# Optimization experiments

Measured on AMD Instinct MI355X. Metric: run time of the kernel, lower is better.

## Reference

```python
import jax, jax.numpy as jnp
import numpy as np

DZ, DA, K, T, BS, H = 32, 16, 3, 128, 512, 128


def setup_inputs() -> dict:
    key = jax.random.key(0)
    ks = jax.random.split(key, 8)
    s = 0.02
    # A/C: identity-like init (as in the torch module) plus small noise, per mixture k and timestep t
    A = jnp.eye(DZ, dtype=jnp.float32) + s * jax.random.normal(ks[0], (K, T, DZ, DZ), jnp.float32)
    C = jnp.eye(DA, DZ, dtype=jnp.float32) + s * jax.random.normal(ks[1], (K, T, DA, DZ), jnp.float32)
    a0 = jnp.zeros((DA,), jnp.float32)
    a = jax.random.normal(ks[2], (BS, T, DA), jnp.float32)

    def lw(k, shape):
        return 0.05 * jax.random.normal(k, shape, jnp.float32)

    Wih0 = lw(ks[3], (4 * H, DA)); Whh0 = lw(ks[4], (4 * H, H))
    bih0 = jnp.zeros((4 * H,), jnp.float32); bhh0 = jnp.zeros((4 * H,), jnp.float32)
    Wih1 = lw(ks[5], (4 * H, H)); Whh1 = lw(ks[6], (4 * H, H))
    bih1 = jnp.zeros((4 * H,), jnp.float32); bhh1 = jnp.zeros((4 * H,), jnp.float32)
    Wlin = lw(ks[7], (K, H)); blin = jnp.zeros((K,), jnp.float32)
    return dict(a=a, A=A, C=C, a0=a0, Wih0=Wih0, Whh0=Whh0, bih0=bih0, bhh0=bhh0,
                Wih1=Wih1, Whh1=Whh1, bih1=bih1, bhh1=bhh1, Wlin=Wlin, blin=blin)


def _lstm_layer(x, Wih, Whh, bih, bhh):
    # x: (bs, L, din) -> (bs, L, H); PyTorch gate order i, f, g, o; zero initial state
    Hd = Whh.shape[1]
    b = bih + bhh

    def step(carry, xt):
        h, c = carry
        g = xt @ Wih.T + h @ Whh.T + b
        i, f, gg, o = jnp.split(g, 4, axis=-1)
        c = jax.nn.sigmoid(f) * c + jax.nn.sigmoid(i) * jnp.tanh(gg)
        h = jax.nn.sigmoid(o) * jnp.tanh(c)
        return (h, c), h

    h0 = jnp.zeros((x.shape[0], Hd), x.dtype)
    _, hs = jax.lax.scan(step, (h0, h0), jnp.swapaxes(x, 0, 1))
    return jnp.swapaxes(hs, 0, 1)


def _filter(a, A, C, a0, Wih0, Whh0, bih0, bhh0, Wih1, Whh1, bih1, bhh1, Wlin, blin):
    bs, L, da = a.shape
    dz = A.shape[-1]
    R = 0.01 * jnp.eye(da, dtype=a.dtype)
    Q = 0.01 * jnp.eye(dz, dtype=a.dtype)

    # dynamics network: alpha_t from [a_0, a_0..a_{L-2}]
    code = jnp.concatenate([jnp.broadcast_to(a0, (bs, 1, da)), a[:, :-1]], axis=1)
    h = _lstm_layer(code, Wih0, Whh0, bih0, bhh0)
    h = _lstm_layer(h, Wih1, Whh1, bih1, bhh1)
    alpha = jax.nn.softmax(h @ Wlin.T + blin, axis=-1)  # (bs, L, K)

    A_mix = jnp.einsum('blk,klij->blij', alpha, A)  # (bs, L, dz, dz)
    C_mix = jnp.einsum('blk,klij->blij', alpha, C)  # (bs, L, da, dz)
    # A is applied at index t+1 for the prediction step; last slot is a dummy (its output is unused)
    A_next = jnp.concatenate([A_mix[:, 1:], A_mix[:, -1:]], axis=1)

    mu0 = jnp.zeros((bs, dz), a.dtype)
    sig0 = jnp.broadcast_to(jnp.eye(dz, dtype=a.dtype), (bs, dz, dz))
    I = jnp.eye(dz, dtype=a.dtype)

    def step(carry, inp):
        mu_pred, sigma_pred = carry
        Ct, At_next, at = inp  # (bs,da,dz), (bs,dz,dz), (bs,da)
        r = at - jnp.einsum('bij,bj->bi', Ct, mu_pred)
        CtT = jnp.swapaxes(Ct, 1, 2)
        S = Ct @ sigma_pred @ CtT + R                      # (bs, da, da)
        Kg = sigma_pred @ CtT @ jnp.linalg.inv(S)          # (bs, dz, da)
        mu = mu_pred + jnp.einsum('bij,bj->bi', Kg, r)
        sigma = (I - Kg @ Ct) @ sigma_pred
        mu_next = jnp.einsum('bij,bj->bi', At_next, mu)
        sigma_next = At_next @ sigma @ jnp.swapaxes(At_next, 1, 2) + Q
        return (mu_next, sigma_next), mu

    xs = (jnp.swapaxes(C_mix, 0, 1), jnp.swapaxes(A_next, 0, 1), jnp.swapaxes(a, 0, 1))
    _, means = jax.lax.scan(step, (mu0, sig0), xs)
    return jnp.swapaxes(means, 0, 1)  # filtered means (bs, L, dz)


def reference(a, A, C, a0, Wih0, Whh0, bih0, bhh0, Wih1, Whh1, bih1, bhh1, Wlin, blin):
    return _filter(a, A, C, a0, Wih0, Whh0, bih0, bhh0,
                   Wih1, Whh1, bih1, bhh1, Wlin, blin)
```

## Files before the change

### kernel.cpp

```cpp
#include <hip/hip_runtime.h>
#include <hip/hip_fp16.h>
#include <cstdint>

#define T_LEN 128
#define DA    16
#define DZ    32
#define HH    128

__device__ __forceinline__ float sigm(float x){ return 1.0f/(1.0f + __expf(-x)); }
__device__ __forceinline__ float tanh_f(float x){ return 1.0f - 2.0f/(__expf(2.0f*x)+1.0f); }
__device__ __forceinline__ float dot4(float4 a, float4 b){ return a.x*b.x + a.y*b.y + a.z*b.z + a.w*b.w; }

typedef _Float16 h2v __attribute__((ext_vector_type(2)));
__device__ __forceinline__ float fdot2(uint32_t w, uint32_t h, float acc){
  union{uint32_t u; h2v v;} a, b; a.u = w; b.u = h;
  return __builtin_amdgcn_fdot2(a.v, b.v, acc, false);
}
__device__ __forceinline__ uint32_t packh2(float x, float y){
  return (uint32_t)__half_as_ushort(__float2half(x)) |
         ((uint32_t)__half_as_ushort(__float2half(y)) << 16);
}


__global__ void prep_kernel(const float* __restrict__ Wih0, const float* __restrict__ Whh0,
                            const float* __restrict__ bih0, const float* __restrict__ bhh0,
                            const float* __restrict__ Wih1, const float* __restrict__ Whh1,
                            const float* __restrict__ bih1, const float* __restrict__ bhh1,
                            uint32_t* __restrict__ ws) {
  int idx = blockIdx.x*256 + threadIdx.x;
  if (idx < 4096) {
    int q = idx & 3, g = (idx >> 2) & 511, m = idx >> 11;
    int k0 = 8*m + 2*q;
    ws[idx] = packh2(Wih0[g*DA + k0], Wih0[g*DA + k0 + 1]);
  } else if (idx < 36864) {
    int f = idx - 4096;
    int q = f & 3, g = (f >> 2) & 511, m = f >> 11;
    int k0 = 8*m + 2*q;
    ws[idx] = packh2(Whh0[g*HH + k0], Whh0[g*HH + k0 + 1]);
  } else if (idx < 69632) {
    int f = idx - 36864;
    int q = f & 3, g = (f >> 2) & 511, m = f >> 11;
    int k0 = 8*m + 2*q;
    ws[idx] = packh2(Wih1[g*HH + k0], Wih1[g*HH + k0 + 1]);
  } else if (idx < 102400) {
    int f = idx - 69632;
    int q = f & 3, g = (f >> 2) & 511, m = f >> 11;
    int k0 = 8*m + 2*q;
    ws[idx] = packh2(Whh1[g*HH + k0], Whh1[g*HH + k0 + 1]);
  } else if (idx < 102912) {
    int j = idx - 102400;
    ((float*)ws)[idx] = bih0[j] + bhh0[j];
  } else if (idx < 103424) {
    int j = idx - 102912;
    ((float*)ws)[idx] = bih1[j] + bhh1[j];
  }
}

__global__ __launch_bounds__(512, 2) void lstm_kernel(
    const float* __restrict__ a, const float* __restrict__ a0,
    const uint32_t* __restrict__ wsw, const float* __restrict__ Wlin,
    const float* __restrict__ blin, float* __restrict__ alpha_out) {
  const uint4* Wih0p = (const uint4*)(wsw);
  const uint4* Whh0p = (const uint4*)(wsw + 4096);
  const uint4* Wih1p = (const uint4*)(wsw + 36864);
  const uint4* Whh1p = (const uint4*)(wsw + 69632);
  const float* b0v = (const float*)(wsw + 102400);
  const float* b1v = (const float*)(wsw + 102912);

  __shared__ __align__(16) uint32_t sxh[2][T_LEN][8];
  __shared__ __align__(16) uint32_t sh0h[2][64];
  __shared__ __align__(16) uint32_t sh1h[2][64];
  __shared__ float gates[2][4*HH];

  int tid = threadIdx.x;
  int lane = tid & 63;
  int wv = tid >> 6;
  int bb = blockIdx.x * 2;

  uint4 wi0[2], wh0[16], wi1[16], wh1[16];
  #pragma unroll
  for (int m = 0; m < 2; ++m)  wi0[m] = Wih0p[m*512 + tid];
  #pragma unroll
  for (int m = 0; m < 16; ++m) wh0[m] = Whh0p[m*512 + tid];
  #pragma unroll
  for (int m = 0; m < 16; ++m) wi1[m] = Wih1p[m*512 + tid];
  #pragma unroll
  for (int m = 0; m < 16; ++m) wh1[m] = Whh1p[m*512 + tid];
  float bi0 = b0v[tid], bi1 = b1v[tid];

  for (int i = tid; i < 2*T_LEN*8; i += 512) {
    int r = i / (T_LEN*8), rem = i % (T_LEN*8), t = rem >> 3, p = rem & 7;
    float x0, x1;
    if (t == 0) { x0 = a0[2*p]; x1 = a0[2*p+1]; }
    else {
      const float* src = a + ((size_t)(bb + r)*T_LEN + (t-1))*DA;
      x0 = src[2*p]; x1 = src[2*p+1];
    }
    sxh[r][t][p] = packh2(x0, x1);
  }
  float wl00 = Wlin[0*HH + 2*lane], wl01 = Wlin[0*HH + 2*lane+1];
  float wl10 = Wlin[1*HH + 2*lane], wl11 = Wlin[1*HH + 2*lane+1];
  float wl20 = Wlin[2*HH + 2*lane], wl21 = Wlin[2*HH + 2*lane+1];
  float bl0 = blin[0], bl1 = blin[1], bl2 = blin[2];
  float c00 = 0.f, c01 = 0.f, c10 = 0.f, c11 = 0.f;
  if (tid < 128) { sh0h[wv][lane] = 0u; sh1h[wv][lane] = 0u; }
  __syncthreads();

  #pragma unroll 1
  for (int t = 0; t < T_LEN; ++t) {
    {
      float g0a = bi0, g0b = 0.f, g1a = bi0, g1b = 0.f;
      uint4 xA0 = *(const uint4*)&sxh[0][t][0];
      uint4 xA1 = *(const uint4*)&sxh[0][t][4];
      uint4 xB0 = *(const uint4*)&sxh[1][t][0];
      uint4 xB1 = *(const uint4*)&sxh[1][t][4];
      g0a = fdot2(wi0[0].x, xA0.x, g0a); g0b = fdot2(wi0[0].y, xA0.y, g0b);
      g0a = fdot2(wi0[0].z, xA0.z, g0a); g0b = fdot2(wi0[0].w, xA0.w, g0b);
      g0a = fdot2(wi0[1].x, xA1.x, g0a); g0b = fdot2(wi0[1].y, xA1.y, g0b);
      g0a = fdot2(wi0[1].z, xA1.z, g0a); g0b = fdot2(wi0[1].w, xA1.w, g0b);
      g1a = fdot2(wi0[0].x, xB0.x, g1a); g1b = fdot2(wi0[0].y, xB0.y, g1b);
      g1a = fdot2(wi0[0].z, xB0.z, g1a); g1b = fdot2(wi0[0].w, xB0.w, g1b);
      g1a = fdot2(wi0[1].x, xB1.x, g1a); g1b = fdot2(wi0[1].y, xB1.y, g1b);
      g1a = fdot2(wi0[1].z, xB1.z, g1a); g1b = fdot2(wi0[1].w, xB1.w, g1b);
      #pragma unroll
      for (int m = 0; m < 16; ++m) {
        uint4 w = wh0[m];
        uint4 hA = *(const uint4*)&sh0h[0][4*m];
        uint4 hB = *(const uint4*)&sh0h[1][4*m];
        g0a = fdot2(w.x, hA.x, g0a); g0b = fdot2(w.y, hA.y, g0b);
        g0a = fdot2(w.z, hA.z, g0a); g0b = fdot2(w.w, hA.w, g0b);
        g1a = fdot2(w.x, hB.x, g1a); g1b = fdot2(w.y, hB.y, g1b);
        g1a = fdot2(w.z, hB.z, g1a); g1b = fdot2(w.w, hB.w, g1b);
      }
      gates[0][tid] = g0a + g0b;
      gates[1][tid] = g1a + g1b;
    }
    __syncthreads();
    if (tid < 128) {
      int j0 = 2*lane, j1 = j0 + 1;
      float i0 = gates[wv][j0],      f0 = gates[wv][j0+HH],
            q0 = gates[wv][j0+2*HH], o0 = gates[wv][j0+3*HH];
      c00 = sigm(f0)*c00 + sigm(i0)*tanh_f(q0);
      float hv0 = sigm(o0)*tanh_f(c00);
      float i1 = gates[wv][j1],      f1 = gates[wv][j1+HH],
            q1 = gates[wv][j1+2*HH], o1 = gates[wv][j1+3*HH];
      c01 = sigm(f1)*c01 + sigm(i1)*tanh_f(q1);
      float hv1 = sigm(o1)*tanh_f(c01);
      sh0h[wv][lane] = packh2(hv0, hv1);
    }
    __syncthreads();
    {
      float g0a = bi1, g0b = 0.f, g1a = bi1, g1b = 0.f;
      #pragma unroll
      for (int m = 0; m < 16; ++m) {
        uint4 w = wi1[m];
        uint4 hA = *(const uint4*)&sh0h[0][4*m];
        uint4 hB = *(const uint4*)&sh0h[1][4*m];
        g0a = fdot2(w.x, hA.x, g0a); g0b = fdot2(w.y, hA.y, g0b);
        g0a = fdot2(w.z, hA.z, g0a); g0b = fdot2(w.w, hA.w, g0b);
        g1a = fdot2(w.x, hB.x, g1a); g1b = fdot2(w.y, hB.y, g1b);
        g1a = fdot2(w.z, hB.z, g1a); g1b = fdot2(w.w, hB.w, g1b);
      }
      #pragma unroll
      for (int m = 0; m < 16; ++m) {
        uint4 w = wh1[m];
        uint4 hA = *(const uint4*)&sh1h[0][4*m];
        uint4 hB = *(const uint4*)&sh1h[1][4*m];
        g0a = fdot2(w.x, hA.x, g0a); g0b = fdot2(w.y, hA.y, g0b);
        g0a = fdot2(w.z, hA.z, g0a); g0b = fdot2(w.w, hA.w, g0b);
        g1a = fdot2(w.x, hB.x, g1a); g1b = fdot2(w.y, hB.y, g1b);
        g1a = fdot2(w.z, hB.z, g1a); g1b = fdot2(w.w, hB.w, g1b);
      }
      gates[0][tid] = g0a + g0b;
      gates[1][tid] = g1a + g1b;
    }
    __syncthreads();
    float hv0 = 0.f, hv1 = 0.f;
    if (tid < 128) {
      int j0 = 2*lane, j1 = j0 + 1;
      float i0 = gates[wv][j0],      f0 = gates[wv][j0+HH],
            q0 = gates[wv][j0+2*HH], o0 = gates[wv][j0+3*HH];
      c10 = sigm(f0)*c10 + sigm(i0)*tanh_f(q0);
      hv0 = sigm(o0)*tanh_f(c10);
      float i1 = gates[wv][j1],      f1 = gates[wv][j1+HH],
            q1 = gates[wv][j1+2*HH], o1 = gates[wv][j1+3*HH];
      c11 = sigm(f1)*c11 + sigm(i1)*tanh_f(q1);
      hv1 = sigm(o1)*tanh_f(c11);
      sh1h[wv][lane] = packh2(hv0, hv1);
    }
    __syncthreads();
    if (tid < 128) {
      float p0 = hv0*wl00 + hv1*wl01;
      float p1 = hv0*wl10 + hv1*wl11;
      float p2 = hv0*wl20 + hv1*wl21;
      #pragma unroll
      for (int off = 32; off > 0; off >>= 1) {
        p0 += __shfl_down(p0, off); p1 += __shfl_down(p1, off); p2 += __shfl_down(p2, off);
      }
      if (lane == 0) {
        float l0 = p0 + bl0, l1 = p1 + bl1, l2 = p2 + bl2;
        float mx = fmaxf(l0, fmaxf(l1, l2));
        float e0=__expf(l0-mx), e1=__expf(l1-mx), e2=__expf(l2-mx);
        float inv = 1.0f/(e0+e1+e2);
        float* dst = alpha_out + (((size_t)(bb+wv))*T_LEN + t)*3;
        dst[0]=e0*inv; dst[1]=e1*inv; dst[2]=e2*inv;
      }
    }
  }
}

__global__ __launch_bounds__(256) void kalman_kernel(
    const float* __restrict__ a, const float* __restrict__ A,
    const float* __restrict__ C, const float* __restrict__ alpha,
    float* __restrict__ out) {
  __shared__ __align__(16) float Sg[DZ][36];
  __shared__ __align__(16) float Am[DZ][36];
  __shared__ __align__(16) float AmT[DZ][36];
  __shared__ __align__(16) float Cm[DA][36];
  __shared__ __align__(16) float Nn[DZ][20];
  __shared__ __align__(16) float NnT[DA][36];
  __shared__ __align__(16) float Aug[DA][36];
  __shared__ __align__(16) float Kg[DZ][20];
  __shared__ __align__(16) float Sp2[DZ][36];
  __shared__ __align__(16) float T2m[DZ][36];
  __shared__ __align__(16) float sa[T_LEN][DA];
  __shared__ float salpha[T_LEN*3];
  __shared__ __align__(16) float muv[DZ], mun[DZ], rv[DA];

  int tid = threadIdx.x;
  int b = blockIdx.x;

  for (int e = tid; e < T_LEN*DA; e += 256) (&sa[0][0])[e] = a[(size_t)b*T_LEN*DA + e];
  for (int e = tid; e < T_LEN*3; e += 256) salpha[e] = alpha[(size_t)b*T_LEN*3 + e];
  for (int e = tid; e < DZ*36; e += 256) (&Sg[0][0])[e] = 0.0f;
  __syncthreads();
  if (tid < DZ) { Sg[tid][tid] = 1.0f; muv[tid] = 0.0f; }

  const int i8 = tid >> 3, jA = tid & 7, jB = jA + 8, j4m = jA * 4;
  const int i16 = tid >> 4, j16 = tid & 15;
  const int iR = tid & 31, j4r = (tid >> 5) * 4;

  const float4* A4 = (const float4*)A;
  const float4* C4 = (const float4*)C;
  float4 pA0 = A4[(0*T_LEN + 1)*256 + tid];
  float4 pA1 = A4[(1*T_LEN + 1)*256 + tid];
  float4 pA2 = A4[(2*T_LEN + 1)*256 + tid];
  float4 pC0, pC1, pC2;
  if (tid < 128) {
    pC0 = C4[(0*T_LEN + 0)*128 + tid];
    pC1 = C4[(1*T_LEN + 0)*128 + tid];
    pC2 = C4[(2*T_LEN + 0)*128 + tid];
  }
  __syncthreads();

  #pragma unroll 1
  for (int t = 0; t < T_LEN; ++t) {
    int ta = (t < T_LEN-1) ? t+1 : t;
    float b10 = salpha[ta*3+0], b11 = salpha[ta*3+1], b12 = salpha[ta*3+2];
    float b00 = salpha[t*3+0],  b01 = salpha[t*3+1],  b02 = salpha[t*3+2];

    {
      float4 v;
      v.x = b10*pA0.x + b11*pA1.x + b12*pA2.x;
      v.y = b10*pA0.y + b11*pA1.y + b12*pA2.y;
      v.z = b10*pA0.z + b11*pA1.z + b12*pA2.z;
      v.w = b10*pA0.w + b11*pA1.w + b12*pA2.w;
      *(float4*)&Am[i8][j4m] = v;
      AmT[j4m+0][i8] = v.x; AmT[j4m+1][i8] = v.y;
      AmT[j4m+2][i8] = v.z; AmT[j4m+3][i8] = v.w;
      if (tid < 128) {
        float4 c;
        c.x = b00*pC0.x + b01*pC1.x + b02*pC2.x;
        c.y = b00*pC0.y + b01*pC1.y + b02*pC2.y;
        c.z = b00*pC0.z + b01*pC1.z + b02*pC2.z;
        c.w = b00*pC0.w + b01*pC1.w + b02*pC2.w;
        *(float4*)&Cm[tid>>3][(tid&7)*4] = c;
      }
      int tn  = (t+1 < T_LEN) ? t+1 : T_LEN-1;
      int tan = (tn < T_LEN-1) ? tn+1 : tn;
      pA0 = A4[(0*T_LEN + tan)*256 + tid];
      pA1 = A4[(1*T_LEN + tan)*256 + tid];
      pA2 = A4[(2*T_LEN + tan)*256 + tid];
      if (tid < 128) {
        pC0 = C4[(0*T_LEN + tn)*128 + tid];
        pC1 = C4[(1*T_LEN + tn)*128 + tid];
        pC2 = C4[(2*T_LEN + tn)*128 + tid];
      }
    }
    __syncthreads();

    {
      float accA = 0.0f, accB = 0.0f;
      #pragma unroll
      for (int k4 = 0; k4 < 8; ++k4) {
        float4 s  = *(const float4*)&Sg[i8][k4*4];
        float4 cA = *(const float4*)&Cm[jA][k4*4];
        float4 cB = *(const float4*)&Cm[jB][k4*4];
        accA += dot4(s,cA); accB += dot4(s,cB);
      }
      Nn[i8][jA] = accA; Nn[i8][jB] = accB;
      NnT[jA][i8] = accA; NnT[jB][i8] = accB;
      if (tid < DA) {
        float acc = sa[t][tid];
        #pragma unroll
        for (int k4 = 0; k4 < 8; ++k4)
          acc -= dot4(*(const float4*)&Cm[tid][k4*4], *(const float4*)&muv[k4*4]);
        rv[tid] = acc;
      }
    }
    __syncthreads();

    {
      float acc = 0.0f;
      #pragma unroll
      for (int k4 = 0; k4 < 8; ++k4) {
        float4 c = *(const float4*)&Cm[i16][k4*4];
        float4 n = *(const float4*)&NnT[j16][k4*4];
        acc += dot4(c,n);
      }
      Aug[i16][j16] = acc + ((i16 == j16) ? 0.01f : 0.0f);
      Aug[i16][16 + j16] = (i16 == j16) ? 1.0f : 0.0f;
    }
    __syncthreads();

    if (tid < 64) {
      int lane = tid;
      int r = lane >> 2, cb = lane & 3;
      float v[8];
      #pragma unroll
      for (int j = 0; j < 8; ++j) v[j] = Aug[r][cb*8 + j];
      #pragma unroll
      for (int p = 0; p < DA; ++p) {
        float App = __shfl(v[p & 7], (p << 2) | (p >> 3), 64);
        float f   = __shfl(v[p & 7], (lane & 60) | (p >> 3), 64);
        float prow[8];
        #pragma unroll
        for (int j = 0; j < 8; ++j) prow[j] = __shfl(v[j], (p << 2) | cb, 64);
        float pinv = 1.0f / App;
        if (r == p) {
          #pragma unroll
          for (int j = 0; j < 8; ++j) v[j] *= pinv;
        } else {
          float fp = f * pinv;
          #pragma unroll
          for (int j = 0; j < 8; ++j) v[j] -= fp * prow[j];
        }
      }
      if (cb >= 2) {
        #pragma unroll
        for (int j = 0; j < 8; ++j) Aug[r][cb*8 + j] = v[j];
      }
    }
    __syncthreads();

    {
      float accA = 0.0f, accB = 0.0f;
      #pragma unroll
      for (int k4 = 0; k4 < 4; ++k4) {
        float4 n  = *(const float4*)&Nn[i8][k4*4];
        float4 sA = *(const float4*)&Aug[jA][16 + k4*4];
        float4 sB = *(const float4*)&Aug[jB][16 + k4*4];
        accA += dot4(n,sA); accB += dot4(n,sB);
      }
      Kg[i8][jA] = accA; Kg[i8][jB] = accB;
    }
    __syncthreads();

    if (tid < DZ) {
      float m = muv[tid];
      #pragma unroll
      for (int k4 = 0; k4 < 4; ++k4)
        m += dot4(*(const float4*)&Kg[tid][k4*4], *(const float4*)&rv[k4*4]);
      mun[tid] = m;
      out[((size_t)b*T_LEN + t)*DZ + tid] = m;
    }
    {
      float4 acc = *(const float4*)&Sg[iR][j4r];
      #pragma unroll
      for (int k4 = 0; k4 < 4; ++k4) {
        float4 kv = *(const float4*)&Kg[iR][k4*4];
        float4 n0 = *(const float4*)&NnT[4*k4+0][j4r];
        float4 n1 = *(const float4*)&NnT[4*k4+1][j4r];
        float4 n2 = *(const float4*)&NnT[4*k4+2][j4r];
        float4 n3 = *(const float4*)&NnT[4*k4+3][j4r];
        acc.x -= kv.x*n0.x + kv.y*n1.x + kv.z*n2.x + kv.w*n3.x;
        acc.y -= kv.x*n0.y + kv.y*n1.y + kv.z*n2.y + kv.w*n3.y;
        acc.z -= kv.x*n0.z + kv.y*n1.z + kv.z*n2.z + kv.w*n3.z;
        acc.w -= kv.x*n0.w + kv.y*n1.w + kv.z*n2.w + kv.w*n3.w;
      }
      *(float4*)&Sp2[iR][j4r] = acc;
    }
    __syncthreads();

    {
      float4 acc = make_float4(0.f,0.f,0.f,0.f);
      #pragma unroll
      for (int k4 = 0; k4 < 8; ++k4) {
        float4 av = *(const float4*)&Am[iR][k4*4];
        float4 b0 = *(const float4*)&Sp2[4*k4+0][j4r];
        float4 b1 = *(const float4*)&Sp2[4*k4+1][j4r];
        float4 b2 = *(const float4*)&Sp2[4*k4+2][j4r];
        float4 b3 = *(const float4*)&Sp2[4*k4+3][j4r];
        acc.x += av.x*b0.x + av.y*b1.x + av.z*b2.x + av.w*b3.x;
        acc.y += av.x*b0.y + av.y*b1.y + av.z*b2.y + av.w*b3.y;
        acc.z += av.x*b0.z + av.y*b1.z + av.z*b2.z + av.w*b3.z;
        acc.w += av.x*b0.w + av.y*b1.w + av.z*b2.w + av.w*b3.w;
      }
      *(float4*)&T2m[iR][j4r] = acc;
    }
    __syncthreads();

    {
      float4 acc = make_float4(0.f,0.f,0.f,0.f);
      #pragma unroll
      for (int k4 = 0; k4 < 8; ++k4) {
        float4 tv = *(const float4*)&T2m[iR][k4*4];
        float4 b0 = *(const float4*)&AmT[4*k4+0][j4r];
        float4 b1 = *(const float4*)&AmT[4*k4+1][j4r];
        float4 b2 = *(const float4*)&AmT[4*k4+2][j4r];
        float4 b3 = *(const float4*)&AmT[4*k4+3][j4r];
        acc.x += tv.x*b0.x + tv.y*b1.x + tv.z*b2.x + tv.w*b3.x;
        acc.y += tv.x*b0.y + tv.y*b1.y + tv.z*b2.y + tv.w*b3.y;
        acc.z += tv.x*b0.z + tv.y*b1.z + tv.z*b2.z + tv.w*b3.z;
        acc.w += tv.x*b0.w + tv.y*b1.w + tv.z*b2.w + tv.w*b3.w;
      }
      int d = iR - j4r;
      if (d >= 0 && d < 4) (&acc.x)[d] += 0.01f;
      *(float4*)&Sg[iR][j4r] = acc;
    }
    if (tid < DZ) {
      float m = 0.0f;
      #pragma unroll
      for (int k4 = 0; k4 < 8; ++k4)
        m += dot4(*(const float4*)&Am[tid][k4*4], *(const float4*)&mun[k4*4]);
      muv[tid] = m;
    }
    __syncthreads();
  }
}

extern "C" void kernel_launch(void* const* d_in, const int* in_sizes, int n_in,
                              void* d_out, int out_size, void* d_ws, size_t ws_size,
                              hipStream_t stream) {
  const float* a    = (const float*)d_in[0];
  const float* A    = (const float*)d_in[1];
  const float* C    = (const float*)d_in[2];
  const float* a0   = (const float*)d_in[3];
  const float* Wih0 = (const float*)d_in[4];
  const float* Whh0 = (const float*)d_in[5];
  const float* bih0 = (const float*)d_in[6];
  const float* bhh0 = (const float*)d_in[7];
  const float* Wih1 = (const float*)d_in[8];
  const float* Whh1 = (const float*)d_in[9];
  const float* bih1 = (const float*)d_in[10];
  const float* bhh1 = (const float*)d_in[11];
  const float* Wlin = (const float*)d_in[12];
  const float* blin = (const float*)d_in[13];
  uint32_t* ws = (uint32_t*)d_ws;
  float* alpha = (float*)(ws + 103424);
  float* out = (float*)d_out;

  prep_kernel<<<404, 256, 0, stream>>>(Wih0, Whh0, bih0, bhh0, Wih1, Whh1, bih1, bhh1, ws);
  lstm_kernel<<<256, 512, 0, stream>>>(a, a0, ws, Wlin, blin, alpha);
  kalman_kernel<<<512, 256, 0, stream>>>(a, A, C, alpha, out);
}
```

Before: 1.258 ms.

## Run Kalman filter per batch on a single wavefront, replacing barriers with LDS waits

The Kalman kernel drops from 256 to 64 threads per block, so each batch element is handled by one wavefront. Every block-wide barrier is replaced by an s_waitcnt lgkmcnt(0), and each thread now computes 4x4 or 2x2 register tiles. The transposed A copy is removed because the A·Σ·Aᵀ product now reads A rows directly. This cuts barrier overhead in the serial time loop, but gives less parallelism per block, and correctness depends on lockstep execution within the wave.

```diff
diff --git a/kernel.cpp b/kernel.cpp
--- a/kernel.cpp
+++ b/kernel.cpp
@@ -20,6 +20,8 @@
   return (uint32_t)__half_as_ushort(__float2half(x)) |
          ((uint32_t)__half_as_ushort(__float2half(y)) << 16);
 }
+
+#define WSYNC() asm volatile("s_waitcnt lgkmcnt(0)" ::: "memory")
 
 
 __global__ void prep_kernel(const float* __restrict__ Wih0, const float* __restrict__ Whh0,
@@ -209,13 +211,12 @@
   }
 }
 
-__global__ __launch_bounds__(256) void kalman_kernel(
+__global__ __launch_bounds__(64, 1) void kalman_kernel(
     const float* __restrict__ a, const float* __restrict__ A,
     const float* __restrict__ C, const float* __restrict__ alpha,
     float* __restrict__ out) {
   __shared__ __align__(16) float Sg[DZ][36];
   __shared__ __align__(16) float Am[DZ][36];
-  __shared__ __align__(16) float AmT[DZ][36];
   __shared__ __align__(16) float Cm[DA][36];
   __shared__ __align__(16) float Nn[DZ][20];
   __shared__ __align__(16) float NnT[DA][36];
@@ -225,114 +226,138 @@
   __shared__ __align__(16) float T2m[DZ][36];
   __shared__ __align__(16) float sa[T_LEN][DA];
   __shared__ float salpha[T_LEN*3];
-  __shared__ __align__(16) float muv[DZ], mun[DZ], rv[DA];
-
-  int tid = threadIdx.x;
-  int b = blockIdx.x;
-
-  for (int e = tid; e < T_LEN*DA; e += 256) (&sa[0][0])[e] = a[(size_t)b*T_LEN*DA + e];
-  for (int e = tid; e < T_LEN*3; e += 256) salpha[e] = alpha[(size_t)b*T_LEN*3 + e];
-  for (int e = tid; e < DZ*36; e += 256) (&Sg[0][0])[e] = 0.0f;
-  __syncthreads();
-  if (tid < DZ) { Sg[tid][tid] = 1.0f; muv[tid] = 0.0f; }
-
-  const int i8 = tid >> 3, jA = tid & 7, jB = jA + 8, j4m = jA * 4;
-  const int i16 = tid >> 4, j16 = tid & 15;
-  const int iR = tid & 31, j4r = (tid >> 5) * 4;
+  __shared__ __align__(16) float muv[DZ];
+  __shared__ __align__(16) float mun[DZ];
+  __shared__ __align__(16) float rv[DA];
+
+  const int l  = threadIdx.x;
+  const int bi = l >> 3;
+  const int bj = l & 7;
+  const int b  = blockIdx.x;
+
+  {
+    const float4* asrc = (const float4*)(a + (size_t)b*T_LEN*DA);
+    float4* adst = (float4*)&sa[0][0];
+    #pragma unroll
+    for (int e = 0; e < 8; ++e) adst[e*64 + l] = asrc[e*64 + l];
+    const float* alsrc = alpha + (size_t)b*T_LEN*3;
+    #pragma unroll
+    for (int e = 0; e < 6; ++e) salpha[e*64 + l] = alsrc[e*64 + l];
+    for (int i = l; i < DZ*36; i += 64) (&Sg[0][0])[i] = 0.0f;
+    if (l < DZ) muv[l] = 0.0f;
+  }
+  WSYNC();
+  if (l < DZ) Sg[l][l] = 1.0f;
+  WSYNC();
 
   const float4* A4 = (const float4*)A;
   const float4* C4 = (const float4*)C;
-  float4 pA0 = A4[(0*T_LEN + 1)*256 + tid];
-  float4 pA1 = A4[(1*T_LEN + 1)*256 + tid];
-  float4 pA2 = A4[(2*T_LEN + 1)*256 + tid];
-  float4 pC0, pC1, pC2;
-  if (tid < 128) {
-    pC0 = C4[(0*T_LEN + 0)*128 + tid];
-    pC1 = C4[(1*T_LEN + 0)*128 + tid];
-    pC2 = C4[(2*T_LEN + 0)*128 + tid];
+
+  float4 pA[3][4], pC[3][2];
+  #pragma unroll
+  for (int k = 0; k < 3; ++k) {
+    #pragma unroll
+    for (int r = 0; r < 4; ++r) pA[k][r] = A4[((k*T_LEN + 1)*DZ + 4*bi + r)*8 + bj];
+    #pragma unroll
+    for (int r = 0; r < 2; ++r) pC[k][r] = C4[((k*T_LEN + 0)*DA + 2*bi + r)*8 + bj];
   }
-  __syncthreads();
 
   #pragma unroll 1
   for (int t = 0; t < T_LEN; ++t) {
-    int ta = (t < T_LEN-1) ? t+1 : t;
-    float b10 = salpha[ta*3+0], b11 = salpha[ta*3+1], b12 = salpha[ta*3+2];
-    float b00 = salpha[t*3+0],  b01 = salpha[t*3+1],  b02 = salpha[t*3+2];
-
-    {
+    const int ta = (t < T_LEN-1) ? t+1 : t;
+    const float b10 = salpha[ta*3+0], b11 = salpha[ta*3+1], b12 = salpha[ta*3+2];
+    const float b00 = salpha[t*3+0],  b01 = salpha[t*3+1],  b02 = salpha[t*3+2];
+
+    #pragma unroll
+    for (int r = 0; r < 4; ++r) {
       float4 v;
-      v.x = b10*pA0.x + b11*pA1.x + b12*pA2.x;
-      v.y = b10*pA0.y + b11*pA1.y + b12*pA2.y;
-      v.z = b10*pA0.z + b11*pA1.z + b12*pA2.z;
-      v.w = b10*pA0.w + b11*pA1.w + b12*pA2.w;
-      *(float4*)&Am[i8][j4m] = v;
-      AmT[j4m+0][i8] = v.x; AmT[j4m+1][i8] = v.y;
-      AmT[j4m+2][i8] = v.z; AmT[j4m+3][i8] = v.w;
-      if (tid < 128) {
-        float4 c;
-        c.x = b00*pC0.x + b01*pC1.x + b02*pC2.x;
-        c.y = b00*pC0.y + b01*pC1.y + b02*pC2.y;
-        c.z = b00*pC0.z + b01*pC1.z + b02*pC2.z;
-        c.w = b00*pC0.w + b01*pC1.w + b02*pC2.w;
-        *(float4*)&Cm[tid>>3][(tid&7)*4] = c;
-      }
-      int tn  = (t+1 < T_LEN) ? t+1 : T_LEN-1;
-      int tan = (tn < T_LEN-1) ? tn+1 : tn;
-      pA0 = A4[(0*T_LEN + tan)*256 + tid];
-      pA1 = A4[(1*T_LEN + tan)*256 + tid];
-      pA2 = A4[(2*T_LEN + tan)*256 + tid];
-      if (tid < 128) {
-        pC0 = C4[(0*T_LEN + tn)*128 + tid];
-        pC1 = C4[(1*T_LEN + tn)*128 + tid];
-        pC2 = C4[(2*T_LEN + tn)*128 + tid];
-      }
-    }
-    __syncthreads();
-
-    {
-      float accA = 0.0f, accB = 0.0f;
+      v.x = b10*pA[0][r].x + b11*pA[1][r].x + b12*pA[2][r].x;
+      v.y = b10*pA[0][r].y + b11*pA[1][r].y + b12*pA[2][r].y;
+      v.z = b10*pA[0][r].z + b11*pA[1][r].z + b12*pA[2][r].z;
+      v.w = b10*pA[0][r].w + b11*pA[1][r].w + b12*pA[2][r].w;
+      *(float4*)&Am[4*bi+r][4*bj] = v;
+    }
+    #pragma unroll
+    for (int r = 0; r < 2; ++r) {
+      float4 c;
+      c.x = b00*pC[0][r].x + b01*pC[1][r].x + b02*pC[2][r].x;
+      c.y = b00*pC[0][r].y + b01*pC[1][r].y + b02*pC[2][r].y;
+      c.z = b00*pC[0][r].z + b01*pC[1][r].z + b02*pC[2][r].z;
+      c.w = b00*pC[0][r].w + b01*pC[1][r].w + b02*pC[2][r].w;
+      *(float4*)&Cm[2*bi+r][4*bj] = c;
+    }
+    {
+      const int tn  = (t+1 < T_LEN) ? t+1 : T_LEN-1;
+      const int tan = (tn < T_LEN-1) ? tn+1 : tn;
+      #pragma unroll
+      for (int k = 0; k < 3; ++k) {
+        #pragma unroll
+        for (int r = 0; r < 4; ++r) pA[k][r] = A4[((k*T_LEN + tan)*DZ + 4*bi + r)*8 + bj];
+        #pragma unroll
+        for (int r = 0; r < 2; ++r) pC[k][r] = C4[((k*T_LEN + tn)*DA + 2*bi + r)*8 + bj];
+      }
+    }
+    WSYNC();
+
+    {
+      float accA[4] = {0.f,0.f,0.f,0.f}, accB[4] = {0.f,0.f,0.f,0.f};
       #pragma unroll
       for (int k4 = 0; k4 < 8; ++k4) {
-        float4 s  = *(const float4*)&Sg[i8][k4*4];
-        float4 cA = *(const float4*)&Cm[jA][k4*4];
-        float4 cB = *(const float4*)&Cm[jB][k4*4];
-        accA += dot4(s,cA); accB += dot4(s,cB);
-      }
-      Nn[i8][jA] = accA; Nn[i8][jB] = accB;
-      NnT[jA][i8] = accA; NnT[jB][i8] = accB;
-      if (tid < DA) {
-        float acc = sa[t][tid];
+        float4 cA = *(const float4*)&Cm[2*bj][4*k4];
+        float4 cB = *(const float4*)&Cm[2*bj+1][4*k4];
+        #pragma unroll
+        for (int r = 0; r < 4; ++r) {
+          float4 s = *(const float4*)&Sg[4*bi+r][4*k4];
+          accA[r] += dot4(s, cA); accB[r] += dot4(s, cB);
+        }
+      }
+      #pragma unroll
+      for (int r = 0; r < 4; ++r)
+        *(float2*)&Nn[4*bi+r][2*bj] = make_float2(accA[r], accB[r]);
+      *(float4*)&NnT[2*bj][4*bi]   = make_float4(accA[0], accA[1], accA[2], accA[3]);
+      *(float4*)&NnT[2*bj+1][4*bi] = make_float4(accB[0], accB[1], accB[2], accB[3]);
+      if (l < DA) {
+        float acc = sa[t][l];
         #pragma unroll
         for (int k4 = 0; k4 < 8; ++k4)
-          acc -= dot4(*(const float4*)&Cm[tid][k4*4], *(const float4*)&muv[k4*4]);
-        rv[tid] = acc;
-      }
-    }
-    __syncthreads();
-
-    {
-      float acc = 0.0f;
+          acc -= dot4(*(const float4*)&Cm[l][4*k4], *(const float4*)&muv[4*k4]);
+        rv[l] = acc;
+      }
+    }
+    WSYNC();
+
+    {
+      float a00=0.f, a01=0.f, a10=0.f, a11=0.f;
       #pragma unroll
       for (int k4 = 0; k4 < 8; ++k4) {
-        float4 c = *(const float4*)&Cm[i16][k4*4];
-        float4 n = *(const float4*)&NnT[j16][k4*4];
-        acc += dot4(c,n);
-      }
-      Aug[i16][j16] = acc + ((i16 == j16) ? 0.01f : 0.0f);
-      Aug[i16][16 + j16] = (i16 == j16) ? 1.0f : 0.0f;
-    }
-    __syncthreads();
-
-    if (tid < 64) {
-      int lane = tid;
-      int r = lane >> 2, cb = lane & 3;
+        float4 c0 = *(const float4*)&Cm[2*bi][4*k4];
+        float4 c1 = *(const float4*)&Cm[2*bi+1][4*k4];
+        float4 n0 = *(const float4*)&NnT[2*bj][4*k4];
+        float4 n1 = *(const float4*)&NnT[2*bj+1][4*k4];
+        a00 += dot4(c0,n0); a01 += dot4(c0,n1);
+        a10 += dot4(c1,n0); a11 += dot4(c1,n1);
+      }
+      const int i0 = 2*bi, j0 = 2*bj;
+      a00 += (i0   == j0  ) ? 0.01f : 0.f;
+      a01 += (i0   == j0+1) ? 0.01f : 0.f;
+      a10 += (i0+1 == j0  ) ? 0.01f : 0.f;
+      a11 += (i0+1 == j0+1) ? 0.01f : 0.f;
+      *(float2*)&Aug[i0][j0]   = make_float2(a00, a01);
+      *(float2*)&Aug[i0+1][j0] = make_float2(a10, a11);
+      *(float2*)&Aug[i0][16+j0]   = make_float2((i0==j0)?1.f:0.f, (i0==j0+1)?1.f:0.f);
+      *(float2*)&Aug[i0+1][16+j0] = make_float2((i0+1==j0)?1.f:0.f, (i0+1==j0+1)?1.f:0.f);
+    }
+    WSYNC();
+
+    {
+      int r = l >> 2, cb = l & 3;
       float v[8];
       #pragma unroll
       for (int j = 0; j < 8; ++j) v[j] = Aug[r][cb*8 + j];
       #pragma unroll
       for (int p = 0; p < DA; ++p) {
         float App = __shfl(v[p & 7], (p << 2) | (p >> 3), 64);
-        float f   = __shfl(v[p & 7], (lane & 60) | (p >> 3), 64);
+        float f   = __shfl(v[p & 7], (l & 60) | (p >> 3), 64);
         float prow[8];
         #pragma unroll
         for (int j = 0; j < 8; ++j) prow[j] = __shfl(v[j], (p << 2) | cb, 64);
@@ -351,91 +376,107 @@
         for (int j = 0; j < 8; ++j) Aug[r][cb*8 + j] = v[j];
       }
     }
-    __syncthreads();
-
-    {
-      float accA = 0.0f, accB = 0.0f;
+    WSYNC();
+
+    {
+      float kA[4] = {0.f,0.f,0.f,0.f}, kB[4] = {0.f,0.f,0.f,0.f};
       #pragma unroll
       for (int k4 = 0; k4 < 4; ++k4) {
-        float4 n  = *(const float4*)&Nn[i8][k4*4];
-        float4 sA = *(const float4*)&Aug[jA][16 + k4*4];
-        float4 sB = *(const float4*)&Aug[jB][16 + k4*4];
-        accA += dot4(n,sA); accB += dot4(n,sB);
-      }
-      Kg[i8][jA] = accA; Kg[i8][jB] = accB;
-    }
-    __syncthreads();
-
-    if (tid < DZ) {
-      float m = muv[tid];
+        float4 siA = *(const float4*)&Aug[2*bj][16+4*k4];
+        float4 siB = *(const float4*)&Aug[2*bj+1][16+4*k4];
+        #pragma unroll
+        for (int r = 0; r < 4; ++r) {
+          float4 n = *(const float4*)&Nn[4*bi+r][4*k4];
+          kA[r] += dot4(n, siA); kB[r] += dot4(n, siB);
+        }
+      }
+      #pragma unroll
+      for (int r = 0; r < 4; ++r)
+        *(float2*)&Kg[4*bi+r][2*bj] = make_float2(kA[r], kB[r]);
+    }
+    WSYNC();
+
+    if (l < DZ) {
+      float m = muv[l];
       #pragma unroll
       for (int k4 = 0; k4 < 4; ++k4)
-        m += dot4(*(const float4*)&Kg[tid][k4*4], *(const float4*)&rv[k4*4]);
-      mun[tid] = m;
-      out[((size_t)b*T_LEN + t)*DZ + tid] = m;
-    }
-    {
-      float4 acc = *(const float4*)&Sg[iR][j4r];
+        m += dot4(*(const float4*)&Kg[l][4*k4], *(const float4*)&rv[4*k4]);
+      mun[l] = m;
+      out[((size_t)b*T_LEN + t)*DZ + l] = m;
+    }
+    {
+      float4 acc[4];
+      #pragma unroll
+      for (int r = 0; r < 4; ++r) acc[r] = *(const float4*)&Sg[4*bi+r][4*bj];
       #pragma unroll
       for (int k4 = 0; k4 < 4; ++k4) {
-        float4 kv = *(const float4*)&Kg[iR][k4*4];
-        float4 n0 = *(const float4*)&NnT[4*k4+0][j4r];
-        float4 n1 = *(const float4*)&NnT[4*k4+1][j4r];
-        float4 n2 = *(const float4*)&NnT[4*k4+2][j4r];
-        float4 n3 = *(const float4*)&NnT[4*k4+3][j4r];
-        acc.x -= kv.x*n0.x + kv.y*n1.x + kv.z*n2.x + kv.w*n3.x;
-        acc.y -= kv.x*n0.y + kv.y*n1.y + kv.z*n2.y + kv.w*n3.y;
-        acc.z -= kv.x*n0.z + kv.y*n1.z + kv.z*n2.z + kv.w*n3.z;
-        acc.w -= kv.x*n0.w + kv.y*n1.w + kv.z*n2.w + kv.w*n3.w;
-      }
-      *(float4*)&Sp2[iR][j4r] = acc;
-    }
-    __syncthreads();
-
-    {
-      float4 acc = make_float4(0.f,0.f,0.f,0.f);
+        float4 n0 = *(const float4*)&Nn[4*bj+0][4*k4];
+        float4 n1 = *(const float4*)&Nn[4*bj+1][4*k4];
+        float4 n2 = *(const float4*)&Nn[4*bj+2][4*k4];
+        float4 n3 = *(const float4*)&Nn[4*bj+3][4*k4];
+        #pragma unroll
+        for (int r = 0; r < 4; ++r) {
+          float4 kg = *(const float4*)&Kg[4*bi+r][4*k4];
+          acc[r].x -= dot4(kg, n0); acc[r].y -= dot4(kg, n1);
+          acc[r].z -= dot4(kg, n2); acc[r].w -= dot4(kg, n3);
+        }
+      }
+      #pragma unroll
+      for (int r = 0; r < 4; ++r) *(float4*)&Sp2[4*bi+r][4*bj] = acc[r];
+    }
+    WSYNC();
+
+    {
+      float4 acc[4] = {{0,0,0,0},{0,0,0,0},{0,0,0,0},{0,0,0,0}};
       #pragma unroll
       for (int k4 = 0; k4 < 8; ++k4) {
-        float4 av = *(const float4*)&Am[iR][k4*4];
-        float4 b0 = *(const float4*)&Sp2[4*k4+0][j4r];
-        float4 b1 = *(const float4*)&Sp2[4*k4+1][j4r];
-        float4 b2 = *(const float4*)&Sp2[4*k4+2][j4r];
-        float4 b3 = *(const float4*)&Sp2[4*k4+3][j4r];
-        acc.x += av.x*b0.x + av.y*b1.x + av.z*b2.x + av.w*b3.x;
-        acc.y += av.x*b0.y + av.y*b1.y + av.z*b2.y + av.w*b3.y;
-        acc.z += av.x*b0.z + av.y*b1.z + av.z*b2.z + av.w*b3.z;
-        acc.w += av.x*b0.w + av.y*b1.w + av.z*b2.w + av.w*b3.w;
-      }
-      *(float4*)&T2m[iR][j4r] = acc;
-    }
-    __syncthreads();
-
-    {
-      float4 acc = make_float4(0.f,0.f,0.f,0.f);
+        float4 sp0 = *(const float4*)&Sp2[4*k4+0][4*bj];
+        float4 sp1 = *(const float4*)&Sp2[4*k4+1][4*bj];
+        float4 sp2v= *(const float4*)&Sp2[4*k4+2][4*bj];
+        float4 sp3 = *(const float4*)&Sp2[4*k4+3][4*bj];
+        #pragma unroll
+        for (int r = 0; r < 4; ++r) {
+          float4 am = *(const float4*)&Am[4*bi+r][4*k4];
+          acc[r].x += am.x*sp0.x + am.y*sp1.x + am.z*sp2v.x + am.w*sp3.x;
+          acc[r].y += am.x*sp0.y + am.y*sp1.y + am.z*sp2v.y + am.w*sp3.y;
+          acc[r].z += am.x*sp0.z + am.y*sp1.z + am.z*sp2v.z + am.w*sp3.z;
+          acc[r].w += am.x*sp0.w + am.y*sp1.w + am.z*sp2v.w + am.w*sp3.w;
+        }
+      }
+      #pragma unroll
+      for (int r = 0; r < 4; ++r) *(float4*)&T2m[4*bi+r][4*bj] = acc[r];
+    }
+    WSYNC();
+
+    {
+      float4 acc[4] = {{0,0,0,0},{0,0,0,0},{0,0,0,0},{0,0,0,0}};
       #pragma unroll
       for (int k4 = 0; k4 < 8; ++k4) {
-        float4 tv = *(const float4*)&T2m[iR][k4*4];
-        float4 b0 = *(const float4*)&AmT[4*k4+0][j4r];
-        float4 b1 = *(const float4*)&AmT[4*k4+1][j4r];
-        float4 b2 = *(const float4*)&AmT[4*k4+2][j4r];
-        float4 b3 = *(const float4*)&AmT[4*k4+3][j4r];
-        acc.x += tv.x*b0.x + tv.y*b1.x + tv.z*b2.x + tv.w*b3.x;
-        acc.y += tv.x*b0.y + tv.y*b1.y + tv.z*b2.y + tv.w*b3.y;
-        acc.z += tv.x*b0.z + tv.y*b1.z + tv.z*b2.z + tv.w*b3.z;
-        acc.w += tv.x*b0.w + tv.y*b1.w + tv.z*b2.w + tv.w*b3.w;
-      }
-      int d = iR - j4r;
-      if (d >= 0 && d < 4) (&acc.x)[d] += 0.01f;
-      *(float4*)&Sg[iR][j4r] = acc;
-    }
-    if (tid < DZ) {
-      float m = 0.0f;
-      #pragma unroll
-      for (int k4 = 0; k4 < 8; ++k4)
-        m += dot4(*(const float4*)&Am[tid][k4*4], *(const float4*)&mun[k4*4]);
-      muv[tid] = m;
-    }
-    __syncthreads();
+        float4 am0 = *(const float4*)&Am[4*bj+0][4*k4];
+        float4 am1 = *(const float4*)&Am[4*bj+1][4*k4];
+        float4 am2 = *(const float4*)&Am[4*bj+2][4*k4];
+        float4 am3 = *(const float4*)&Am[4*bj+3][4*k4];
+        #pragma unroll
+        for (int r = 0; r < 4; ++r) {
+          float4 t2 = *(const float4*)&T2m[4*bi+r][4*k4];
+          acc[r].x += dot4(t2, am0); acc[r].y += dot4(t2, am1);
+          acc[r].z += dot4(t2, am2); acc[r].w += dot4(t2, am3);
+        }
+      }
+      if (bi == bj) {
+        acc[0].x += 0.01f; acc[1].y += 0.01f; acc[2].z += 0.01f; acc[3].w += 0.01f;
+      }
+      #pragma unroll
+      for (int r = 0; r < 4; ++r) *(float4*)&Sg[4*bi+r][4*bj] = acc[r];
+      if (l < DZ) {
+        float m = 0.0f;
+        #pragma unroll
+        for (int k4 = 0; k4 < 8; ++k4)
+          m += dot4(*(const float4*)&Am[l][4*k4], *(const float4*)&mun[4*k4]);
+        muv[l] = m;
+      }
+    }
+    WSYNC();
   }
 }
 
@@ -462,5 +503,5 @@
 
   prep_kernel<<<404, 256, 0, stream>>>(Wih0, Whh0, bih0, bhh0, Wih1, Whh1, bih1, bhh1, ws);
   lstm_kernel<<<256, 512, 0, stream>>>(a, a0, ws, Wlin, blin, alpha);
-  kalman_kernel<<<512, 256, 0, stream>>>(a, A, C, alpha, out);
+  kalman_kernel<<<512, 64, 0, stream>>>(a, A, C, alpha, out);
 }
```

Result: slower. 1.565 ms (+24.4%).

## Restructure Kalman covariance update to shorten serial barrier chain

Applied to the files above, without the earlier changes.

Reorders the Kalman step algebra: A·Σ and A·Σ·Aᵀ are computed in parallel with the innovation covariance, and the posterior covariance comes from G − (A·K)·(A·Σ·Cᵀ)ᵀ instead of three chained 32×32 products. The Kalman-gain mean update is folded into the inverse stage via S⁻¹r, and each timestep drops from eight barriers to six. It also swaps __syncthreads for a raw waitcnt plus s_barrier and sets launch bounds to two blocks per CU. In exchange there is extra arithmetic per step and a different floating-point ordering.

```diff
diff --git a/kernel.cpp b/kernel.cpp
--- a/kernel.cpp
+++ b/kernel.cpp
@@ -20,6 +20,9 @@
   return (uint32_t)__half_as_ushort(__float2half(x)) |
          ((uint32_t)__half_as_ushort(__float2half(y)) << 16);
 }
+
+#define BAR() do { asm volatile("s_waitcnt lgkmcnt(0)" ::: "memory"); \
+                   __builtin_amdgcn_s_barrier(); } while (0)
 
 
 __global__ void prep_kernel(const float* __restrict__ Wih0, const float* __restrict__ Whh0,
@@ -209,23 +212,24 @@
   }
 }
 
-__global__ __launch_bounds__(256) void kalman_kernel(
+__global__ __launch_bounds__(256, 2) void kalman_kernel(
     const float* __restrict__ a, const float* __restrict__ A,
     const float* __restrict__ C, const float* __restrict__ alpha,
     float* __restrict__ out) {
   __shared__ __align__(16) float Sg[DZ][36];
   __shared__ __align__(16) float Am[DZ][36];
-  __shared__ __align__(16) float AmT[DZ][36];
   __shared__ __align__(16) float Cm[DA][36];
+  __shared__ __align__(16) float AmSg[DZ][36];
+  __shared__ __align__(16) float Gm[DZ][36];
   __shared__ __align__(16) float Nn[DZ][20];
   __shared__ __align__(16) float NnT[DA][36];
+  __shared__ __align__(16) float Mm[DZ][20];
   __shared__ __align__(16) float Aug[DA][36];
   __shared__ __align__(16) float Kg[DZ][20];
-  __shared__ __align__(16) float Sp2[DZ][36];
-  __shared__ __align__(16) float T2m[DZ][36];
+  __shared__ __align__(16) float AKg[DZ][20];
   __shared__ __align__(16) float sa[T_LEN][DA];
   __shared__ float salpha[T_LEN*3];
-  __shared__ __align__(16) float muv[DZ], mun[DZ], rv[DA];
+  __shared__ __align__(16) float muv[DZ], mun[DZ], rv[DA], wv[DA];
 
   int tid = threadIdx.x;
   int b = blockIdx.x;
@@ -266,8 +270,6 @@
       v.z = b10*pA0.z + b11*pA1.z + b12*pA2.z;
       v.w = b10*pA0.w + b11*pA1.w + b12*pA2.w;
       *(float4*)&Am[i8][j4m] = v;
-      AmT[j4m+0][i8] = v.x; AmT[j4m+1][i8] = v.y;
-      AmT[j4m+2][i8] = v.z; AmT[j4m+3][i8] = v.w;
       if (tid < 128) {
         float4 c;
         c.x = b00*pC0.x + b01*pC1.x + b02*pC2.x;
@@ -287,41 +289,79 @@
         pC2 = C4[(2*T_LEN + tn)*128 + tid];
       }
     }
-    __syncthreads();
-
-    {
+    BAR();
+
+    {
+      float4 acc = make_float4(0.f,0.f,0.f,0.f);
+      #pragma unroll
+      for (int k4 = 0; k4 < 8; ++k4) {
+        float4 am = *(const float4*)&Am[iR][4*k4];
+        float4 s0 = *(const float4*)&Sg[4*k4+0][j4r];
+        float4 s1 = *(const float4*)&Sg[4*k4+1][j4r];
+        float4 s2 = *(const float4*)&Sg[4*k4+2][j4r];
+        float4 s3 = *(const float4*)&Sg[4*k4+3][j4r];
+        acc.x += am.x*s0.x + am.y*s1.x + am.z*s2.x + am.w*s3.x;
+        acc.y += am.x*s0.y + am.y*s1.y + am.z*s2.y + am.w*s3.y;
+        acc.z += am.x*s0.z + am.y*s1.z + am.z*s2.z + am.w*s3.z;
+        acc.w += am.x*s0.w + am.y*s1.w + am.z*s2.w + am.w*s3.w;
+      }
+      *(float4*)&AmSg[iR][j4r] = acc;
+
       float accA = 0.0f, accB = 0.0f;
       #pragma unroll
       for (int k4 = 0; k4 < 8; ++k4) {
-        float4 s  = *(const float4*)&Sg[i8][k4*4];
-        float4 cA = *(const float4*)&Cm[jA][k4*4];
-        float4 cB = *(const float4*)&Cm[jB][k4*4];
+        float4 s  = *(const float4*)&Sg[i8][4*k4];
+        float4 cA = *(const float4*)&Cm[jA][4*k4];
+        float4 cB = *(const float4*)&Cm[jB][4*k4];
         accA += dot4(s,cA); accB += dot4(s,cB);
       }
       Nn[i8][jA] = accA; Nn[i8][jB] = accB;
       NnT[jA][i8] = accA; NnT[jB][i8] = accB;
       if (tid < DA) {
-        float acc = sa[t][tid];
+        float acc2 = sa[t][tid];
         #pragma unroll
         for (int k4 = 0; k4 < 8; ++k4)
-          acc -= dot4(*(const float4*)&Cm[tid][k4*4], *(const float4*)&muv[k4*4]);
-        rv[tid] = acc;
-      }
-    }
-    __syncthreads();
-
-    {
-      float acc = 0.0f;
+          acc2 -= dot4(*(const float4*)&Cm[tid][4*k4], *(const float4*)&muv[4*k4]);
+        rv[tid] = acc2;
+      }
+    }
+    BAR();
+
+    {
+      float4 acc = make_float4(0.f,0.f,0.f,0.f);
       #pragma unroll
       for (int k4 = 0; k4 < 8; ++k4) {
-        float4 c = *(const float4*)&Cm[i16][k4*4];
-        float4 n = *(const float4*)&NnT[j16][k4*4];
-        acc += dot4(c,n);
-      }
-      Aug[i16][j16] = acc + ((i16 == j16) ? 0.01f : 0.0f);
+        float4 p  = *(const float4*)&AmSg[iR][4*k4];
+        float4 a0v = *(const float4*)&Am[j4r+0][4*k4];
+        float4 a1v = *(const float4*)&Am[j4r+1][4*k4];
+        float4 a2v = *(const float4*)&Am[j4r+2][4*k4];
+        float4 a3v = *(const float4*)&Am[j4r+3][4*k4];
+        acc.x += dot4(p,a0v); acc.y += dot4(p,a1v);
+        acc.z += dot4(p,a2v); acc.w += dot4(p,a3v);
+      }
+      *(float4*)&Gm[iR][j4r] = acc;
+
+      float mA = 0.0f, mB = 0.0f;
+      #pragma unroll
+      for (int k4 = 0; k4 < 8; ++k4) {
+        float4 p  = *(const float4*)&AmSg[i8][4*k4];
+        float4 cA = *(const float4*)&Cm[jA][4*k4];
+        float4 cB = *(const float4*)&Cm[jB][4*k4];
+        mA += dot4(p,cA); mB += dot4(p,cB);
+      }
+      Mm[i8][jA] = mA; Mm[i8][jB] = mB;
+
+      float acc2 = 0.0f;
+      #pragma unroll
+      for (int k4 = 0; k4 < 8; ++k4) {
+        float4 c = *(const float4*)&Cm[i16][4*k4];
+        float4 n = *(const float4*)&NnT[j16][4*k4];
+        acc2 += dot4(c,n);
+      }
+      Aug[i16][j16] = acc2 + ((i16 == j16) ? 0.01f : 0.0f);
       Aug[i16][16 + j16] = (i16 == j16) ? 1.0f : 0.0f;
     }
-    __syncthreads();
+    BAR();
 
     if (tid < 64) {
       int lane = tid;
@@ -346,96 +386,69 @@
           for (int j = 0; j < 8; ++j) v[j] -= fp * prow[j];
         }
       }
+      float part = 0.0f;
       if (cb >= 2) {
         #pragma unroll
         for (int j = 0; j < 8; ++j) Aug[r][cb*8 + j] = v[j];
-      }
-    }
-    __syncthreads();
-
-    {
-      float accA = 0.0f, accB = 0.0f;
+        int c0 = (cb - 2) * 8;
+        float4 r0 = *(const float4*)&rv[c0];
+        float4 r1 = *(const float4*)&rv[c0 + 4];
+        part = v[0]*r0.x + v[1]*r0.y + v[2]*r0.z + v[3]*r0.w
+             + v[4]*r1.x + v[5]*r1.y + v[6]*r1.z + v[7]*r1.w;
+      }
+      part += __shfl_xor(part, 1, 64);
+      if (cb == 2) wv[r] = part;
+    }
+    BAR();
+
+    {
+      float kA = 0.0f, kB = 0.0f, qA = 0.0f, qB = 0.0f;
       #pragma unroll
       for (int k4 = 0; k4 < 4; ++k4) {
-        float4 n  = *(const float4*)&Nn[i8][k4*4];
-        float4 sA = *(const float4*)&Aug[jA][16 + k4*4];
-        float4 sB = *(const float4*)&Aug[jB][16 + k4*4];
-        accA += dot4(n,sA); accB += dot4(n,sB);
-      }
-      Kg[i8][jA] = accA; Kg[i8][jB] = accB;
-    }
-    __syncthreads();
-
-    if (tid < DZ) {
-      float m = muv[tid];
-      #pragma unroll
-      for (int k4 = 0; k4 < 4; ++k4)
-        m += dot4(*(const float4*)&Kg[tid][k4*4], *(const float4*)&rv[k4*4]);
-      mun[tid] = m;
-      out[((size_t)b*T_LEN + t)*DZ + tid] = m;
-    }
-    {
-      float4 acc = *(const float4*)&Sg[iR][j4r];
+        float4 siA = *(const float4*)&Aug[jA][16 + 4*k4];
+        float4 siB = *(const float4*)&Aug[jB][16 + 4*k4];
+        float4 n   = *(const float4*)&Nn[i8][4*k4];
+        float4 m   = *(const float4*)&Mm[i8][4*k4];
+        kA += dot4(n,siA); kB += dot4(n,siB);
+        qA += dot4(m,siA); qB += dot4(m,siB);
+      }
+      Kg[i8][jA] = kA; Kg[i8][jB] = kB;
+      AKg[i8][jA] = qA; AKg[i8][jB] = qB;
+      if (tid < DZ) {
+        float mval = muv[tid];
+        #pragma unroll
+        for (int k4 = 0; k4 < 4; ++k4)
+          mval += dot4(*(const float4*)&Nn[tid][4*k4], *(const float4*)&wv[4*k4]);
+        mun[tid] = mval;
+        out[((size_t)b*T_LEN + t)*DZ + tid] = mval;
+      }
+    }
+    BAR();
+
+    {
+      float4 acc = *(const float4*)&Gm[iR][j4r];
       #pragma unroll
       for (int k4 = 0; k4 < 4; ++k4) {
-        float4 kv = *(const float4*)&Kg[iR][k4*4];
-        float4 n0 = *(const float4*)&NnT[4*k4+0][j4r];
-        float4 n1 = *(const float4*)&NnT[4*k4+1][j4r];
-        float4 n2 = *(const float4*)&NnT[4*k4+2][j4r];
-        float4 n3 = *(const float4*)&NnT[4*k4+3][j4r];
-        acc.x -= kv.x*n0.x + kv.y*n1.x + kv.z*n2.x + kv.w*n3.x;
-        acc.y -= kv.x*n0.y + kv.y*n1.y + kv.z*n2.y + kv.w*n3.y;
-        acc.z -= kv.x*n0.z + kv.y*n1.z + kv.z*n2.z + kv.w*n3.z;
-        acc.w -= kv.x*n0.w + kv.y*n1.w + kv.z*n2.w + kv.w*n3.w;
-      }
-      *(float4*)&Sp2[iR][j4r] = acc;
-    }
-    __syncthreads();
-
-    {
-      float4 acc = make_float4(0.f,0.f,0.f,0.f);
-      #pragma unroll
-      for (int k4 = 0; k4 < 8; ++k4) {
-        float4 av = *(const float4*)&Am[iR][k4*4];
-        float4 b0 = *(const float4*)&Sp2[4*k4+0][j4r];
-        float4 b1 = *(const float4*)&Sp2[4*k4+1][j4r];
-        float4 b2 = *(const float4*)&Sp2[4*k4+2][j4r];
-        float4 b3 = *(const float4*)&Sp2[4*k4+3][j4r];
-        acc.x += av.x*b0.x + av.y*b1.x + av.z*b2.x + av.w*b3.x;
-        acc.y += av.x*b0.y + av.y*b1.y + av.z*b2.y + av.w*b3.y;
-        acc.z += av.x*b0.z + av.y*b1.z + av.z*b2.z + av.w*b3.z;
-        acc.w += av.x*b0.w + av.y*b1.w + av.z*b2.w + av.w*b3.w;
-      }
-      *(float4*)&T2m[iR][j4r] = acc;
-    }
-    __syncthreads();
-
-    {
-      float4 acc = make_float4(0.f,0.f,0.f,0.f);
-      #pragma unroll
-      for (int k4 = 0; k4 < 8; ++k4) {
-        float4 tv = *(const float4*)&T2m[iR][k4*4];
-        float4 b0 = *(const float4*)&AmT[4*k4+0][j4r];
-        float4 b1 = *(const float4*)&AmT[4*k4+1][j4r];
-        float4 b2 = *(const float4*)&AmT[4*k4+2][j4r];
-        float4 b3 = *(const float4*)&AmT[4*k4+3][j4r];
-        acc.x += tv.x*b0.x + tv.y*b1.x + tv.z*b2.x + tv.w*b3.x;
-        acc.y += tv.x*b0.y + tv.y*b1.y + tv.z*b2.y + tv.w*b3.y;
-        acc.z += tv.x*b0.z + tv.y*b1.z + tv.z*b2.z + tv.w*b3.z;
-        acc.w += tv.x*b0.w + tv.y*b1.w + tv.z*b2.w + tv.w*b3.w;
+        float4 kq = *(const float4*)&AKg[iR][4*k4];
+        float4 m0 = *(const float4*)&Mm[j4r+0][4*k4];
+        float4 m1 = *(const float4*)&Mm[j4r+1][4*k4];
+        float4 m2 = *(const float4*)&Mm[j4r+2][4*k4];
+        float4 m3 = *(const float4*)&Mm[j4r+3][4*k4];
+        acc.x -= dot4(kq,m0); acc.y -= dot4(kq,m1);
+        acc.z -= dot4(kq,m2); acc.w -= dot4(kq,m3);
       }
       int d = iR - j4r;
       if (d >= 0 && d < 4) (&acc.x)[d] += 0.01f;
       *(float4*)&Sg[iR][j4r] = acc;
-    }
-    if (tid < DZ) {
-      float m = 0.0f;
-      #pragma unroll
-      for (int k4 = 0; k4 < 8; ++k4)
-        m += dot4(*(const float4*)&Am[tid][k4*4], *(const float4*)&mun[k4*4]);
-      muv[tid] = m;
-    }
-    __syncthreads();
+      if (tid < DZ) {
+        float mval = 0.0f;
+        #pragma unroll
+        for (int k4 = 0; k4 < 8; ++k4)
+          mval += dot4(*(const float4*)&Am[tid][4*k4], *(const float4*)&mun[4*k4]);
+        muv[tid] = mval;
+      }
+    }
+    BAR();
   }
 }
 
```

New measurement: 1.392 ms. 10.7% more time.
